# Kernel optimization log

Measured on AMD Instinct MI355X. Metric: run time of the kernel, lower is better.

## Reference

```python
import jax, jax.numpy as jnp
import numpy as np
from functools import partial

IM_H, IM_W = 1024, 1024
PRE_NMS = 1000
POST_NMS = 1000
FPN_POST_NMS = 1000
NMS_THRESH = 0.7
MIN_SIZE = 0.0
XFORM_CLIP = float(np.log(1000.0 / 16.0))  # BoxCoder bbox_xform_clip
K_MIN, K_MAX, K0, S0 = 2, 5, 4, 224.0      # ROI->FPN level mapper
NEG_INF = -1.0e30
N_IMG = 8


def _make_anchors(H, W, stride, n_img):
    """Grid anchors in H,W,A order (matches permute(0,2,3,1) flattening)."""
    ratios = np.array([0.5, 1.0, 2.0])
    size = stride * 8.0
    ws = size * np.sqrt(1.0 / ratios)
    hs = size * np.sqrt(ratios)
    sx = (np.arange(W) + 0.5) * stride
    sy = (np.arange(H) + 0.5) * stride
    cx, cy = np.meshgrid(sx, sy)  # [H,W]
    x1 = cx[..., None] - ws / 2.0
    y1 = cy[..., None] - hs / 2.0
    x2 = cx[..., None] + ws / 2.0
    y2 = cy[..., None] + hs / 2.0
    anc = np.stack([x1, y1, x2, y2], -1).reshape(-1, 4).astype(np.float32)
    return jnp.asarray(np.broadcast_to(anc, (n_img,) + anc.shape).copy())


def setup_inputs() -> dict:
    key = jax.random.key(0)
    ks = jax.random.split(key, 6)
    inp = {
        "obj_p2": jax.random.normal(ks[0], (N_IMG, 3, 256, 256), jnp.float32),
        "obj_p3": jax.random.normal(ks[1], (N_IMG, 3, 128, 128), jnp.float32),
        "obj_p4": jax.random.normal(ks[2], (N_IMG, 3, 64, 64), jnp.float32),
        "breg_p2": jax.random.normal(ks[3], (N_IMG, 12, 256, 256), jnp.float32) * 0.25,
        "breg_p3": jax.random.normal(ks[4], (N_IMG, 12, 128, 128), jnp.float32) * 0.25,
        "breg_p4": jax.random.normal(ks[5], (N_IMG, 12, 64, 64), jnp.float32) * 0.25,
        "anchors_p2": _make_anchors(256, 256, 4, N_IMG),
        "anchors_p3": _make_anchors(128, 128, 8, N_IMG),
        "anchors_p4": _make_anchors(64, 64, 16, N_IMG),
    }
    return inp


def _decode(deltas, anchors):
    # BoxCoder(weights=(1,1,1,1)) decode with the detectron +1 convention
    w = anchors[..., 2] - anchors[..., 0] + 1.0
    h = anchors[..., 3] - anchors[..., 1] + 1.0
    cx = anchors[..., 0] + 0.5 * w
    cy = anchors[..., 1] + 0.5 * h
    dx, dy = deltas[..., 0], deltas[..., 1]
    dw = jnp.minimum(deltas[..., 2], XFORM_CLIP)
    dh = jnp.minimum(deltas[..., 3], XFORM_CLIP)
    pcx = dx * w + cx
    pcy = dy * h + cy
    pw = jnp.exp(dw) * w
    ph = jnp.exp(dh) * h
    return jnp.stack(
        [pcx - 0.5 * pw, pcy - 0.5 * ph, pcx + 0.5 * pw - 1.0, pcy + 0.5 * ph - 1.0], -1
    )


def _nms_keep(boxes, valid, thresh):
    # boxes [K,4] already sorted by score desc; greedy hard NMS -> keep mask
    x1, y1, x2, y2 = boxes[:, 0], boxes[:, 1], boxes[:, 2], boxes[:, 3]
    areas = (x2 - x1 + 1.0) * (y2 - y1 + 1.0)
    xx1 = jnp.maximum(x1[:, None], x1[None, :])
    yy1 = jnp.maximum(y1[:, None], y1[None, :])
    xx2 = jnp.minimum(x2[:, None], x2[None, :])
    yy2 = jnp.minimum(y2[:, None], y2[None, :])
    inter = jnp.clip(xx2 - xx1 + 1.0, 0.0) * jnp.clip(yy2 - yy1 + 1.0, 0.0)
    iou = inter / (areas[:, None] + areas[None, :] - inter)
    K = boxes.shape[0]
    js = jnp.arange(K)

    def body(i, keep):
        sup = keep[i] & (iou[i] > thresh) & (js > i)
        return keep & ~sup

    return jax.lax.fori_loop(0, K, body, valid)


def _per_level(obj, breg, anchors):
    N, A, H, W = obj.shape
    scores = jax.nn.sigmoid(obj.transpose(0, 2, 3, 1).reshape(N, -1))  # [N, HWA]
    deltas = breg.reshape(N, A, 4, H, W).transpose(0, 3, 4, 1, 2).reshape(N, -1, 4)
    k = min(PRE_NMS, scores.shape[1])
    s, idx = jax.lax.top_k(scores, k)  # sorted desc
    d = jnp.take_along_axis(deltas, idx[..., None], axis=1)
    a = jnp.take_along_axis(anchors, idx[..., None], axis=1)
    p = _decode(d, a)
    # clip to image (width-1 / height-1)
    p = jnp.stack(
        [
            jnp.clip(p[..., 0], 0.0, IM_W - 1.0),
            jnp.clip(p[..., 1], 0.0, IM_H - 1.0),
            jnp.clip(p[..., 2], 0.0, IM_W - 1.0),
            jnp.clip(p[..., 3], 0.0, IM_H - 1.0),
        ],
        -1,
    )
    ws = p[..., 2] - p[..., 0] + 1.0
    hs = p[..., 3] - p[..., 1] + 1.0
    xc = p[..., 0] + ws / 2.0
    yc = p[..., 1] + hs / 2.0
    valid = (ws >= MIN_SIZE) & (hs >= MIN_SIZE) & (xc < IM_W) & (yc < IM_H)
    keep = jax.vmap(partial(_nms_keep, thresh=NMS_THRESH))(p, valid)
    ms = jnp.where(keep, s, NEG_INF)
    s2, i2 = jax.lax.top_k(ms, min(POST_NMS, k))
    b2 = jnp.take_along_axis(p, i2[..., None], axis=1)
    return b2, s2


def reference(obj_p2, obj_p3, obj_p4, breg_p2, breg_p3, breg_p4,
              anchors_p2, anchors_p3, anchors_p4):
    levels_in = [
        (obj_p2, breg_p2, anchors_p2),
        (obj_p3, breg_p3, anchors_p3),
        (obj_p4, breg_p4, anchors_p4),
    ]
    bs, ss = zip(*[_per_level(o, b, a) for o, b, a in levels_in])
    boxes = jnp.concatenate(bs, axis=1)   # [N, L*POST_NMS, 4]
    scores = jnp.concatenate(ss, axis=1)  # [N, L*POST_NMS]
    pk = min(FPN_POST_NMS, scores.shape[1])
    fs, fi = jax.lax.top_k(scores, pk)    # per-image inference-mode topk
    fb = jnp.take_along_axis(boxes, fi[..., None], axis=1)
    # ROI -> FPN level mapping
    area = (fb[..., 2] - fb[..., 0] + 1.0) * (fb[..., 3] - fb[..., 1] + 1.0)
    lvl = jnp.floor(K0 + jnp.log2(jnp.sqrt(area) / S0 + 1e-6))
    lvl = jnp.clip(lvl, K_MIN, K_MAX).astype(jnp.int32)
    return fb, fs, lvl
```

## Files before the change

### kernel.cpp

```cpp
#include <hip/hip_runtime.h>

#define NTASK 24
#define KSEL 1000
#define NIMG 8
#define NEG_INF_D (-1e30)
#define SEG 192
#define SORTN 2048


static __device__ __forceinline__ unsigned fkey(float x) {
    unsigned u = __float_as_uint(x);
    return u ^ ((u >> 31) ? 0xFFFFFFFFu : 0x80000000u);
}

static __device__ __forceinline__ float fkey_inv(unsigned key) {
    unsigned u = (key >> 31) ? (key ^ 0x80000000u) : ~key;
    return __uint_as_float(u);
}

static __device__ __forceinline__ unsigned long long dkey(double d) {
    unsigned long long u = (unsigned long long)__double_as_longlong(d);
    if (u >> 63) u = ~u; else u |= 0x8000000000000000ull;
    return u;
}

static __device__ __forceinline__ int level_hw(int lvl) {
    return lvl == 0 ? 65536 : (lvl == 1 ? 16384 : 4096);
}


__global__ __launch_bounds__(256) void k_zero(uint4* __restrict__ p, int n16) {
    const int t = blockIdx.x * 256 + threadIdx.x;
    if (t < n16) p[t] = make_uint4(0u, 0u, 0u, 0u);
}


__global__ __launch_bounds__(256) void k_hist(const float* __restrict__ o2,
                                              const float* __restrict__ o3,
                                              const float* __restrict__ o4,
                                              unsigned* __restrict__ hist) {
    const int task = blockIdx.x, img = task / 3, lvl = task % 3;
    const float* obj = lvl == 0 ? o2 : (lvl == 1 ? o3 : o4);
    const int HW = level_hw(lvl);
    const int total = 3 * HW;
    const float* base = obj + (size_t)img * total;
    const int tid = threadIdx.x;

    __shared__ unsigned h[4096];
    for (int t = tid; t < 4096; t += 256) h[t] = 0u;
    __syncthreads();

    const int per4 = (total / 32) >> 2;
    const int beg4 = blockIdx.y * per4;
    const float4* base4 = (const float4*)base;
    for (int t = beg4 + tid; t < beg4 + per4; t += 256) {
        float4 v = base4[t];
        atomicAdd(&h[fkey(v.x) >> 20], 1u);
        atomicAdd(&h[fkey(v.y) >> 20], 1u);
        atomicAdd(&h[fkey(v.z) >> 20], 1u);
        atomicAdd(&h[fkey(v.w) >> 20], 1u);
    }
    __syncthreads();

    unsigned* H = hist + task * 4096;
    for (int t = tid; t < 4096; t += 256)
        if (h[t]) atomicAdd(&H[t], h[t]);
}


__global__ __launch_bounds__(256) void k_compact(const float* __restrict__ o2,
                                                 const float* __restrict__ o3,
                                                 const float* __restrict__ o4,
                                                 const unsigned* __restrict__ hist,
                                                 int* __restrict__ cntB,
                                                 unsigned long long* __restrict__ cand) {
    const int task = blockIdx.x, img = task / 3, lvl = task % 3;
    const float* obj = lvl == 0 ? o2 : (lvl == 1 ? o3 : o4);
    const int HW = level_hw(lvl);
    const int total = 3 * HW;
    const float* base = obj + (size_t)img * total;
    const int tid = threadIdx.x;

    __shared__ unsigned h[4096];
    __shared__ unsigned part[256];
    __shared__ int sBin;
    __shared__ unsigned long long buf[256];
    __shared__ unsigned scnt;

    const unsigned* H = hist + task * 4096;
    for (int t = tid; t < 4096; t += 256) h[t] = H[t];
    if (tid == 0) scnt = 0u;
    __syncthreads();
    unsigned sacc = 0;
    for (int q = 0; q < 16; ++q) sacc += h[tid * 16 + q];
    part[tid] = sacc;
    __syncthreads();
    if (tid == 0) {
        unsigned cum = 0;
        int c = 255;
        for (; c >= 0; --c) {
            if (cum + part[c] >= (unsigned)KSEL) break;
            cum += part[c];
        }
        if (c < 0) c = 0;
        int bin = 0;
        for (int b = c * 16 + 15; b >= c * 16; --b) {
            if (cum + h[b] >= (unsigned)KSEL) { bin = b; break; }
            cum += h[b];
        }
        sBin = bin;
    }
    __syncthreads();
    const unsigned B = (unsigned)sBin;

    const int per4 = (total / 32) >> 2;
    const int beg4 = blockIdx.y * per4;
    const float4* base4 = (const float4*)base;
    for (int t = beg4 + tid; t < beg4 + per4; t += 256) {
        float4 v = base4[t];
        const int e0 = t * 4;
#pragma unroll
        for (int q = 0; q < 4; ++q) {
            float x = q == 0 ? v.x : (q == 1 ? v.y : (q == 2 ? v.z : v.w));
            unsigned key = fkey(x);
            if ((key >> 20) >= B) {
                unsigned s = atomicAdd(&scnt, 1u);
                if (s < 256u) {
                    int el = e0 + q;
                    int a = el / HW, pos = el - a * HW;
                    int i = pos * 3 + a;
                    buf[s] = ((unsigned long long)key << 32) | (unsigned)(~(unsigned)i);
                }
            }
        }
    }
    __syncthreads();
    int n = (int)scnt; if (n > SEG) n = SEG;
    const int seg = task * 32 + blockIdx.y;
    if (tid == 0) cntB[seg] = n;
    unsigned long long* C = cand + (size_t)seg * SEG;
    for (int t = tid; t < n; t += 256) C[t] = buf[t];
}


__global__ __launch_bounds__(1024) void k_sel(const int* __restrict__ cntB,
                                              const unsigned long long* __restrict__ cand,
                                              unsigned long long* __restrict__ sorted64) {
    const int task = blockIdx.x, tid = threadIdx.x;
    const int wid = tid >> 6, lane = tid & 63;
    __shared__ unsigned long long comp[SORTN];
    __shared__ int pref[33];

    if (tid == 0) {
        int p = 0;
        for (int s = 0; s < 32; ++s) { pref[s] = p; p += cntB[task * 32 + s]; }
        pref[32] = p;
    }
    for (int t = tid; t < SORTN; t += 1024) comp[t] = 0ull;
    __syncthreads();

    for (int s = wid; s < 32; s += 16) {
        const int b = pref[s], n = pref[s + 1] - b;
        const unsigned long long* C = cand + (size_t)(task * 32 + s) * SEG;
        for (int k = lane; k < n; k += 64)
            if (b + k < SORTN) comp[b + k] = C[k];
    }
    __syncthreads();

    for (unsigned k = 2; k <= SORTN; k <<= 1) {
        for (unsigned j = k >> 1; j > 0; j >>= 1) {
            for (unsigned i = tid; i < SORTN; i += 1024) {
                unsigned ixj = i ^ j;
                if (ixj > i) {
                    unsigned long long A = comp[i], Bv = comp[ixj];
                    bool desc = ((i & k) == 0);
                    if ((A < Bv) == desc) { comp[i] = Bv; comp[ixj] = A; }
                }
            }
            __syncthreads();
        }
    }

    for (int t = tid; t < KSEL; t += 1024) sorted64[task * KSEL + t] = comp[t];
}


__global__ __launch_bounds__(128) void k_decode(
    const unsigned long long* __restrict__ sorted64,
    const float* __restrict__ g2, const float* __restrict__ g3, const float* __restrict__ g4,
    const float* __restrict__ a2, const float* __restrict__ a3, const float* __restrict__ a4,
    double* __restrict__ boxes, double* __restrict__ score, int* __restrict__ valid) {

    const int task = blockIdx.x, img = task / 3, lvl = task % 3;
    const int r = blockIdx.y * 125 + threadIdx.x;
    if (threadIdx.x >= 125) return;

    const float* brg = lvl == 0 ? g2 : (lvl == 1 ? g3 : g4);
    const float* anc = lvl == 0 ? a2 : (lvl == 1 ? a3 : a4);
    const int HW = level_hw(lvl);
    const int N = HW * 3;
    const double XC = 4.135166556742356;

    unsigned long long e = sorted64[task * KSEL + r];
    unsigned key = (unsigned)(e >> 32);
    int i = (int)(~(unsigned)(e & 0xFFFFFFFFull));
    int a = i % 3, pos = i / 3;

    double x = (double)fkey_inv(key);
    double s = 1.0 / (1.0 + exp(-x));

    const float* bb = brg + (size_t)img * 12 * HW + (size_t)(a * 4) * HW + pos;
    double dx = (double)bb[0];
    double dy = (double)bb[(size_t)HW];
    double dw = (double)bb[(size_t)2 * HW];
    double dh = (double)bb[(size_t)3 * HW];

    const float* an = anc + ((size_t)img * N + (size_t)i) * 4;
    double ax1 = an[0], ay1 = an[1], ax2 = an[2], ay2 = an[3];

    double w = ax2 - ax1 + 1.0, h = ay2 - ay1 + 1.0;
    double cx = ax1 + 0.5 * w, cy = ay1 + 0.5 * h;
    if (dw > XC) dw = XC;
    if (dh > XC) dh = XC;
    double pcx = dx * w + cx, pcy = dy * h + cy;
    double pw = exp(dw) * w, ph = exp(dh) * h;
    double x1 = pcx - 0.5 * pw, y1 = pcy - 0.5 * ph;
    double x2 = pcx + 0.5 * pw - 1.0, y2 = pcy + 0.5 * ph - 1.0;
    x1 = fmin(fmax(x1, 0.0), 1023.0);
    y1 = fmin(fmax(y1, 0.0), 1023.0);
    x2 = fmin(fmax(x2, 0.0), 1023.0);
    y2 = fmin(fmax(y2, 0.0), 1023.0);
    double ws_ = x2 - x1 + 1.0, hs_ = y2 - y1 + 1.0;
    double xc = x1 + ws_ / 2.0, yc = y1 + hs_ / 2.0;
    int v = (ws_ >= 0.0) && (hs_ >= 0.0) && (xc < 1024.0) && (yc < 1024.0);

    double* bo = boxes + (size_t)(task * KSEL + r) * 4;
    bo[0] = x1; bo[1] = y1; bo[2] = x2; bo[3] = y2;
    score[task * KSEL + r] = s;
    valid[task * KSEL + r] = v;
}


__global__ __launch_bounds__(512) void k_mask(const double* __restrict__ boxes,
                                              unsigned long long* __restrict__ maskT) {
    const int task = blockIdx.x;
    const int wid = threadIdx.x >> 6, lane = threadIdx.x & 63;
    const int t = blockIdx.y * 8 + wid;
    if (t >= 136) return;
    int I = 0, rem = t;
    while (rem >= 16 - I) { rem -= 16 - I; ++I; }
    const int J = I + rem;

    const double* B = boxes + (size_t)task * KSEL * 4;
    const int j = J * 64 + lane;
    const int jc = j < KSEL ? j : KSEL - 1;
    double jx1 = B[jc * 4 + 0], jy1 = B[jc * 4 + 1];
    double jx2 = B[jc * 4 + 2], jy2 = B[jc * 4 + 3];
    double aj = (jx2 - jx1 + 1.0) * (jy2 - jy1 + 1.0);

    unsigned long long* MT = maskT + (size_t)task * 16000 + (size_t)J * KSEL;
    int iend = I * 64 + 64; if (iend > KSEL) iend = KSEL;
    for (int i = I * 64; i < iend; ++i) {
        double ix1 = B[i * 4 + 0], iy1 = B[i * 4 + 1];
        double ix2 = B[i * 4 + 2], iy2 = B[i * 4 + 3];
        double ai = (ix2 - ix1 + 1.0) * (iy2 - iy1 + 1.0);
        double xx1 = fmax(ix1, jx1), yy1 = fmax(iy1, jy1);
        double xx2 = fmin(ix2, jx2), yy2 = fmin(iy2, jy2);
        double iw = xx2 - xx1 + 1.0; iw = iw > 0.0 ? iw : 0.0;
        double ih = yy2 - yy1 + 1.0; ih = ih > 0.0 ? ih : 0.0;
        double inter = iw * ih;
        double iou = inter / (ai + aj - inter);
        bool sup = (j > i) && (j < KSEL) && (iou > 0.7);
        unsigned long long m = __ballot(sup);
        if (lane == 0) MT[i] = m;
    }
}


__global__ __launch_bounds__(1024) void k_nms(const unsigned long long* __restrict__ maskT,
                                              const int* __restrict__ valid,
                                              const double* __restrict__ score,
                                              int* __restrict__ order, double* __restrict__ s2) {
    const int task = blockIdx.x;
    const int tid = threadIdx.x;
    const int wid = tid >> 6, lane = tid & 63;

    __shared__ unsigned long long Msh[16000];
    __shared__ unsigned long long kws[16];
    __shared__ int prefK[16], prefN[16], totKsh;

    {
        const ulonglong2* MG = (const ulonglong2*)(maskT + (size_t)task * 16000);
        ulonglong2* ML = (ulonglong2*)Msh;
        for (int t = tid; t < 8000; t += 1024) ML[t] = MG[t];
    }
    if (tid < 16) kws[tid] = 0ull;
    __syncthreads();
    if (tid < KSEL && valid[task * KSEL + tid])
        atomicOr(&kws[tid >> 6], 1ull << (tid & 63));
    __syncthreads();

    for (int p = 0; p < 16; ++p) {
        if (p > 0 && wid >= p) {
            unsigned long long kp = kws[p - 1];
            unsigned long long m = ((kp >> lane) & 1ull) ? Msh[wid * KSEL + (p - 1) * 64 + lane] : 0ull;
            if (m) atomicAnd(&kws[wid], ~m);
        }
        if (wid == p) {
            __threadfence_block();
            const int row = p * 64 + lane;
            unsigned long long m = (row < KSEL) ? Msh[p * KSEL + row] : 0ull;
            unsigned long long k = kws[p];
            unsigned long long processed = 0ull;
            while (true) {
                unsigned long long sup = __ballot((m & k) != 0ull);
                unsigned long long rem = k & sup & ~processed;
                if (!rem) break;
                int b = __ffsll((long long)rem) - 1;
                unsigned lo = (unsigned)__builtin_amdgcn_readlane((int)(unsigned)(m & 0xFFFFFFFFull), b);
                unsigned hi = (unsigned)__builtin_amdgcn_readlane((int)(unsigned)(m >> 32), b);
                unsigned long long vict = ((unsigned long long)hi << 32) | lo;
                k &= ~vict;
                processed = (1ull << b) | ((1ull << b) - 1ull);
            }
            if (lane == 0) kws[p] = k;
        }
        __syncthreads();
    }

    if (tid == 0) {
        int pk = 0, pn = 0;
        for (int l = 0; l < 16; ++l) {
            prefK[l] = pk; prefN[l] = pn;
            int limit = KSEL - 64 * l; if (limit > 64) limit = 64;
            int kb = (int)__popcll(kws[l]);
            pk += kb; pn += limit - kb;
        }
        totKsh = pk;
    }
    __syncthreads();

    if (tid < 16) {
        unsigned long long kw = kws[tid];
        int limit = KSEL - 64 * tid; if (limit > 64) limit = 64;
        int ck = prefK[tid], cn = totKsh + prefN[tid];
        for (int b = 0; b < limit; ++b) {
            int jj = tid * 64 + b;
            if ((kw >> b) & 1ull) {
                order[task * KSEL + ck] = jj;
                s2[task * KSEL + ck] = score[task * KSEL + jj];
                ++ck;
            } else {
                order[task * KSEL + cn] = jj;
                s2[task * KSEL + cn] = NEG_INF_D;
                ++cn;
            }
        }
    }
}


__global__ __launch_bounds__(1024) void k_final(const double* __restrict__ boxes,
                                                const double* __restrict__ s2,
                                                const int* __restrict__ order,
                                                float* __restrict__ out) {
    const int img = blockIdx.x;
    const int tid = threadIdx.x;
    __shared__ unsigned long long Mkey[KSEL];
    __shared__ int Mid[KSEL];

    const double* L0 = s2 + (size_t)(img * 3 + 0) * KSEL;
    const double* L1 = s2 + (size_t)(img * 3 + 1) * KSEL;
    const double* L2 = s2 + (size_t)(img * 3 + 2) * KSEL;

    if (tid < KSEL) {
        const int r = tid;
        int lo = 0, hi = r;
        while (lo < hi) {
            int a = (lo + hi) >> 1;
            if (dkey(L0[a]) >= dkey(L1[r - 1 - a])) lo = a + 1; else hi = a;
        }
        int a = lo, b = r - a;
        unsigned long long ka = dkey(L0[a]), kb = dkey(L1[b]);
        if (ka >= kb) { Mkey[r] = ka; Mid[r] = a; }
        else          { Mkey[r] = kb; Mid[r] = 1000 + b; }
    }
    __syncthreads();

    if (tid < KSEL) {
        const int r = tid;
        int lo = 0, hi = r;
        while (lo < hi) {
            int a = (lo + hi) >> 1;
            if (Mkey[a] >= dkey(L2[r - 1 - a])) lo = a + 1; else hi = a;
        }
        int a = lo, b = r - a;
        int e;
        if (a < KSEL && Mkey[a] >= dkey(L2[b])) e = Mid[a];
        else e = 2000 + b;

        int l = e / 1000, rr = e - l * 1000;
        int task = img * 3 + l;
        int pos = order[task * KSEL + rr];
        const double* bo = boxes + (size_t)(task * KSEL + pos) * 4;
        double b0 = bo[0], b1 = bo[1], b2 = bo[2], b3 = bo[3];
        double s = s2[task * KSEL + rr];

        float* fb = out + ((size_t)img * KSEL + r) * 4;
        fb[0] = (float)b0; fb[1] = (float)b1; fb[2] = (float)b2; fb[3] = (float)b3;
        out[8 * KSEL * 4 + img * KSEL + r] = (float)s;

        double area = (b2 - b0 + 1.0) * (b3 - b1 + 1.0);
        double lv = floor(4.0 + log2(sqrt(area) / 224.0 + 1e-6));
        if (!(lv >= 2.0)) lv = 2.0;
        if (lv > 5.0) lv = 5.0;
        out[8 * KSEL * 5 + img * KSEL + r] = (float)lv;
    }
}


extern "C" void kernel_launch(void* const* d_in, const int* in_sizes, int n_in,
                              void* d_out, int out_size, void* d_ws, size_t ws_size,
                              hipStream_t stream) {
    const float* o2 = (const float*)d_in[0];
    const float* o3 = (const float*)d_in[1];
    const float* o4 = (const float*)d_in[2];
    const float* g2 = (const float*)d_in[3];
    const float* g3 = (const float*)d_in[4];
    const float* g4 = (const float*)d_in[5];
    const float* a2 = (const float*)d_in[6];
    const float* a3 = (const float*)d_in[7];
    const float* a4 = (const float*)d_in[8];

    char* ws = (char*)d_ws;
    int*                valid = (int*)(ws + 96000);
    double*             score = (double*)(ws + 192000);
    double*             boxes = (double*)(ws + 384000);
    int*                order = (int*)(ws + 1152000);
    double*             s2    = (double*)(ws + 1248000);
    char*               scr   = ws + 1440000;

    unsigned long long* sorted64 = (unsigned long long*)(ws + 1152000);

    unsigned*           hist  = (unsigned*)(scr + 0);
    int*                cntB  = (int*)(scr + 393216);
    unsigned long long* cand  = (unsigned long long*)(scr + 396288);
    unsigned long long* maskT = (unsigned long long*)scr;

    k_zero<<<96, 256, 0, stream>>>((uint4*)scr, 24576);

    k_hist<<<dim3(NTASK, 32), 256, 0, stream>>>(o2, o3, o4, hist);
    k_compact<<<dim3(NTASK, 32), 256, 0, stream>>>(o2, o3, o4, hist, cntB, cand);
    k_sel<<<NTASK, 1024, 0, stream>>>(cntB, cand, sorted64);
    k_decode<<<dim3(NTASK, 8), 128, 0, stream>>>(sorted64, g2, g3, g4, a2, a3, a4,
                                                 boxes, score, valid);
    k_mask<<<dim3(NTASK, 17), 512, 0, stream>>>(boxes, maskT);
    k_nms<<<NTASK, 1024, 0, stream>>>(maskT, valid, score, order, s2);
    k_final<<<NIMG, 1024, 0, stream>>>(boxes, s2, order, (float*)d_out);
}
```

Baseline: 115.3 us.

## Fuse all pipeline stages into one cooperative persistent kernel with grid syncs

Replaces eight separate kernel launches (zero, histogram, compact, select/sort, decode, IoU mask, NMS, final merge) with a single cooperative kernel of 240 blocks of 1024 threads, separated by grid-wide syncs. The goal is to remove per-launch overhead and inter-kernel gaps, which are a large share of this latency-bound pipeline. The cost is that stages with little parallelism (NMS, final merge) use only a few blocks while the rest sit idle. Grid syncs also carry their own cost, and the large 1024-thread blocks with about 128KB of shared memory limit occupancy in the streaming stages.

```diff
diff --git a/kernel.cpp b/kernel.cpp
--- a/kernel.cpp
+++ b/kernel.cpp
@@ -1,4 +1,7 @@
 #include <hip/hip_runtime.h>
+#include <hip/hip_cooperative_groups.h>
+
+namespace cg = cooperative_groups;
 
 #define NTASK 24
 #define KSEL 1000
@@ -6,6 +9,7 @@
 #define NEG_INF_D (-1e30)
 #define SEG 192
 #define SORTN 2048
+#define NBLK 240
 
 
 static __device__ __forceinline__ unsigned fkey(float x) {
@@ -29,392 +33,393 @@
 }
 
 
-__global__ __launch_bounds__(256) void k_zero(uint4* __restrict__ p, int n16) {
-    const int t = blockIdx.x * 256 + threadIdx.x;
-    if (t < n16) p[t] = make_uint4(0u, 0u, 0u, 0u);
-}
-
-
-__global__ __launch_bounds__(256) void k_hist(const float* __restrict__ o2,
-                                              const float* __restrict__ o3,
-                                              const float* __restrict__ o4,
-                                              unsigned* __restrict__ hist) {
-    const int task = blockIdx.x, img = task / 3, lvl = task % 3;
-    const float* obj = lvl == 0 ? o2 : (lvl == 1 ? o3 : o4);
-    const int HW = level_hw(lvl);
-    const int total = 3 * HW;
-    const float* base = obj + (size_t)img * total;
-    const int tid = threadIdx.x;
-
-    __shared__ unsigned h[4096];
-    for (int t = tid; t < 4096; t += 256) h[t] = 0u;
-    __syncthreads();
-
-    const int per4 = (total / 32) >> 2;
-    const int beg4 = blockIdx.y * per4;
-    const float4* base4 = (const float4*)base;
-    for (int t = beg4 + tid; t < beg4 + per4; t += 256) {
-        float4 v = base4[t];
-        atomicAdd(&h[fkey(v.x) >> 20], 1u);
-        atomicAdd(&h[fkey(v.y) >> 20], 1u);
-        atomicAdd(&h[fkey(v.z) >> 20], 1u);
-        atomicAdd(&h[fkey(v.w) >> 20], 1u);
-    }
-    __syncthreads();
-
-    unsigned* H = hist + task * 4096;
-    for (int t = tid; t < 4096; t += 256)
-        if (h[t]) atomicAdd(&H[t], h[t]);
-}
-
-
-__global__ __launch_bounds__(256) void k_compact(const float* __restrict__ o2,
-                                                 const float* __restrict__ o3,
-                                                 const float* __restrict__ o4,
-                                                 const unsigned* __restrict__ hist,
-                                                 int* __restrict__ cntB,
-                                                 unsigned long long* __restrict__ cand) {
-    const int task = blockIdx.x, img = task / 3, lvl = task % 3;
-    const float* obj = lvl == 0 ? o2 : (lvl == 1 ? o3 : o4);
-    const int HW = level_hw(lvl);
-    const int total = 3 * HW;
-    const float* base = obj + (size_t)img * total;
-    const int tid = threadIdx.x;
-
-    __shared__ unsigned h[4096];
-    __shared__ unsigned part[256];
-    __shared__ int sBin;
-    __shared__ unsigned long long buf[256];
-    __shared__ unsigned scnt;
-
-    const unsigned* H = hist + task * 4096;
-    for (int t = tid; t < 4096; t += 256) h[t] = H[t];
-    if (tid == 0) scnt = 0u;
-    __syncthreads();
-    unsigned sacc = 0;
-    for (int q = 0; q < 16; ++q) sacc += h[tid * 16 + q];
-    part[tid] = sacc;
-    __syncthreads();
-    if (tid == 0) {
-        unsigned cum = 0;
-        int c = 255;
-        for (; c >= 0; --c) {
-            if (cum + part[c] >= (unsigned)KSEL) break;
-            cum += part[c];
-        }
-        if (c < 0) c = 0;
-        int bin = 0;
-        for (int b = c * 16 + 15; b >= c * 16; --b) {
-            if (cum + h[b] >= (unsigned)KSEL) { bin = b; break; }
-            cum += h[b];
-        }
-        sBin = bin;
-    }
-    __syncthreads();
-    const unsigned B = (unsigned)sBin;
-
-    const int per4 = (total / 32) >> 2;
-    const int beg4 = blockIdx.y * per4;
-    const float4* base4 = (const float4*)base;
-    for (int t = beg4 + tid; t < beg4 + per4; t += 256) {
-        float4 v = base4[t];
-        const int e0 = t * 4;
-#pragma unroll
-        for (int q = 0; q < 4; ++q) {
-            float x = q == 0 ? v.x : (q == 1 ? v.y : (q == 2 ? v.z : v.w));
-            unsigned key = fkey(x);
-            if ((key >> 20) >= B) {
-                unsigned s = atomicAdd(&scnt, 1u);
-                if (s < 256u) {
-                    int el = e0 + q;
-                    int a = el / HW, pos = el - a * HW;
-                    int i = pos * 3 + a;
-                    buf[s] = ((unsigned long long)key << 32) | (unsigned)(~(unsigned)i);
-                }
-            }
-        }
-    }
-    __syncthreads();
-    int n = (int)scnt; if (n > SEG) n = SEG;
-    const int seg = task * 32 + blockIdx.y;
-    if (tid == 0) cntB[seg] = n;
-    unsigned long long* C = cand + (size_t)seg * SEG;
-    for (int t = tid; t < n; t += 256) C[t] = buf[t];
-}
-
-
-__global__ __launch_bounds__(1024) void k_sel(const int* __restrict__ cntB,
-                                              const unsigned long long* __restrict__ cand,
-                                              unsigned long long* __restrict__ sorted64) {
-    const int task = blockIdx.x, tid = threadIdx.x;
-    const int wid = tid >> 6, lane = tid & 63;
-    __shared__ unsigned long long comp[SORTN];
-    __shared__ int pref[33];
-
-    if (tid == 0) {
-        int p = 0;
-        for (int s = 0; s < 32; ++s) { pref[s] = p; p += cntB[task * 32 + s]; }
-        pref[32] = p;
-    }
-    for (int t = tid; t < SORTN; t += 1024) comp[t] = 0ull;
-    __syncthreads();
-
-    for (int s = wid; s < 32; s += 16) {
-        const int b = pref[s], n = pref[s + 1] - b;
-        const unsigned long long* C = cand + (size_t)(task * 32 + s) * SEG;
-        for (int k = lane; k < n; k += 64)
-            if (b + k < SORTN) comp[b + k] = C[k];
-    }
-    __syncthreads();
-
-    for (unsigned k = 2; k <= SORTN; k <<= 1) {
-        for (unsigned j = k >> 1; j > 0; j >>= 1) {
-            for (unsigned i = tid; i < SORTN; i += 1024) {
-                unsigned ixj = i ^ j;
-                if (ixj > i) {
-                    unsigned long long A = comp[i], Bv = comp[ixj];
-                    bool desc = ((i & k) == 0);
-                    if ((A < Bv) == desc) { comp[i] = Bv; comp[ixj] = A; }
-                }
-            }
-            __syncthreads();
-        }
-    }
-
-    for (int t = tid; t < KSEL; t += 1024) sorted64[task * KSEL + t] = comp[t];
-}
-
-
-__global__ __launch_bounds__(128) void k_decode(
-    const unsigned long long* __restrict__ sorted64,
+__global__ __launch_bounds__(1024) void k_mega(
+    const float* __restrict__ o2, const float* __restrict__ o3, const float* __restrict__ o4,
     const float* __restrict__ g2, const float* __restrict__ g3, const float* __restrict__ g4,
     const float* __restrict__ a2, const float* __restrict__ a3, const float* __restrict__ a4,
-    double* __restrict__ boxes, double* __restrict__ score, int* __restrict__ valid) {
-
-    const int task = blockIdx.x, img = task / 3, lvl = task % 3;
-    const int r = blockIdx.y * 125 + threadIdx.x;
-    if (threadIdx.x >= 125) return;
-
-    const float* brg = lvl == 0 ? g2 : (lvl == 1 ? g3 : g4);
-    const float* anc = lvl == 0 ? a2 : (lvl == 1 ? a3 : a4);
-    const int HW = level_hw(lvl);
-    const int N = HW * 3;
-    const double XC = 4.135166556742356;
-
-    unsigned long long e = sorted64[task * KSEL + r];
-    unsigned key = (unsigned)(e >> 32);
-    int i = (int)(~(unsigned)(e & 0xFFFFFFFFull));
-    int a = i % 3, pos = i / 3;
-
-    double x = (double)fkey_inv(key);
-    double s = 1.0 / (1.0 + exp(-x));
-
-    const float* bb = brg + (size_t)img * 12 * HW + (size_t)(a * 4) * HW + pos;
-    double dx = (double)bb[0];
-    double dy = (double)bb[(size_t)HW];
-    double dw = (double)bb[(size_t)2 * HW];
-    double dh = (double)bb[(size_t)3 * HW];
-
-    const float* an = anc + ((size_t)img * N + (size_t)i) * 4;
-    double ax1 = an[0], ay1 = an[1], ax2 = an[2], ay2 = an[3];
-
-    double w = ax2 - ax1 + 1.0, h = ay2 - ay1 + 1.0;
-    double cx = ax1 + 0.5 * w, cy = ay1 + 0.5 * h;
-    if (dw > XC) dw = XC;
-    if (dh > XC) dh = XC;
-    double pcx = dx * w + cx, pcy = dy * h + cy;
-    double pw = exp(dw) * w, ph = exp(dh) * h;
-    double x1 = pcx - 0.5 * pw, y1 = pcy - 0.5 * ph;
-    double x2 = pcx + 0.5 * pw - 1.0, y2 = pcy + 0.5 * ph - 1.0;
-    x1 = fmin(fmax(x1, 0.0), 1023.0);
-    y1 = fmin(fmax(y1, 0.0), 1023.0);
-    x2 = fmin(fmax(x2, 0.0), 1023.0);
-    y2 = fmin(fmax(y2, 0.0), 1023.0);
-    double ws_ = x2 - x1 + 1.0, hs_ = y2 - y1 + 1.0;
-    double xc = x1 + ws_ / 2.0, yc = y1 + hs_ / 2.0;
-    int v = (ws_ >= 0.0) && (hs_ >= 0.0) && (xc < 1024.0) && (yc < 1024.0);
-
-    double* bo = boxes + (size_t)(task * KSEL + r) * 4;
-    bo[0] = x1; bo[1] = y1; bo[2] = x2; bo[3] = y2;
-    score[task * KSEL + r] = s;
-    valid[task * KSEL + r] = v;
-}
-
-
-__global__ __launch_bounds__(512) void k_mask(const double* __restrict__ boxes,
-                                              unsigned long long* __restrict__ maskT) {
-    const int task = blockIdx.x;
-    const int wid = threadIdx.x >> 6, lane = threadIdx.x & 63;
-    const int t = blockIdx.y * 8 + wid;
-    if (t >= 136) return;
-    int I = 0, rem = t;
-    while (rem >= 16 - I) { rem -= 16 - I; ++I; }
-    const int J = I + rem;
-
-    const double* B = boxes + (size_t)task * KSEL * 4;
-    const int j = J * 64 + lane;
-    const int jc = j < KSEL ? j : KSEL - 1;
-    double jx1 = B[jc * 4 + 0], jy1 = B[jc * 4 + 1];
-    double jx2 = B[jc * 4 + 2], jy2 = B[jc * 4 + 3];
-    double aj = (jx2 - jx1 + 1.0) * (jy2 - jy1 + 1.0);
-
-    unsigned long long* MT = maskT + (size_t)task * 16000 + (size_t)J * KSEL;
-    int iend = I * 64 + 64; if (iend > KSEL) iend = KSEL;
-    for (int i = I * 64; i < iend; ++i) {
-        double ix1 = B[i * 4 + 0], iy1 = B[i * 4 + 1];
-        double ix2 = B[i * 4 + 2], iy2 = B[i * 4 + 3];
-        double ai = (ix2 - ix1 + 1.0) * (iy2 - iy1 + 1.0);
-        double xx1 = fmax(ix1, jx1), yy1 = fmax(iy1, jy1);
-        double xx2 = fmin(ix2, jx2), yy2 = fmin(iy2, jy2);
-        double iw = xx2 - xx1 + 1.0; iw = iw > 0.0 ? iw : 0.0;
-        double ih = yy2 - yy1 + 1.0; ih = ih > 0.0 ? ih : 0.0;
-        double inter = iw * ih;
-        double iou = inter / (ai + aj - inter);
-        bool sup = (j > i) && (j < KSEL) && (iou > 0.7);
-        unsigned long long m = __ballot(sup);
-        if (lane == 0) MT[i] = m;
-    }
-}
-
-
-__global__ __launch_bounds__(1024) void k_nms(const unsigned long long* __restrict__ maskT,
-                                              const int* __restrict__ valid,
-                                              const double* __restrict__ score,
-                                              int* __restrict__ order, double* __restrict__ s2) {
-    const int task = blockIdx.x;
+    unsigned* __restrict__ hist, int* __restrict__ cntB, unsigned long long* __restrict__ cand,
+    unsigned long long* __restrict__ sorted64,
+    double* __restrict__ boxes, double* __restrict__ score, int* __restrict__ valid,
+    unsigned long long* __restrict__ maskT,
+    int* __restrict__ order, double* __restrict__ s2v,
+    float* __restrict__ out) {
+
+    cg::grid_group grid = cg::this_grid();
     const int tid = threadIdx.x;
-    const int wid = tid >> 6, lane = tid & 63;
-
-    __shared__ unsigned long long Msh[16000];
-    __shared__ unsigned long long kws[16];
-    __shared__ int prefK[16], prefN[16], totKsh;
+    const int bid = blockIdx.x;
+
+    __shared__ unsigned long long U64[16000];
+    __shared__ unsigned long long kwsS[16];
+    __shared__ int prefK[16], prefN[16];
+    __shared__ int prefS[33];
+    __shared__ unsigned scntS;
+    __shared__ int sBin, totK;
 
     {
-        const ulonglong2* MG = (const ulonglong2*)(maskT + (size_t)task * 16000);
-        ulonglong2* ML = (ulonglong2*)Msh;
-        for (int t = tid; t < 8000; t += 1024) ML[t] = MG[t];
-    }
-    if (tid < 16) kws[tid] = 0ull;
-    __syncthreads();
-    if (tid < KSEL && valid[task * KSEL + tid])
-        atomicOr(&kws[tid >> 6], 1ull << (tid & 63));
-    __syncthreads();
-
-    for (int p = 0; p < 16; ++p) {
-        if (p > 0 && wid >= p) {
-            unsigned long long kp = kws[p - 1];
-            unsigned long long m = ((kp >> lane) & 1ull) ? Msh[wid * KSEL + (p - 1) * 64 + lane] : 0ull;
-            if (m) atomicAnd(&kws[wid], ~m);
-        }
-        if (wid == p) {
-            __threadfence_block();
-            const int row = p * 64 + lane;
-            unsigned long long m = (row < KSEL) ? Msh[p * KSEL + row] : 0ull;
-            unsigned long long k = kws[p];
-            unsigned long long processed = 0ull;
-            while (true) {
-                unsigned long long sup = __ballot((m & k) != 0ull);
-                unsigned long long rem = k & sup & ~processed;
-                if (!rem) break;
-                int b = __ffsll((long long)rem) - 1;
-                unsigned lo = (unsigned)__builtin_amdgcn_readlane((int)(unsigned)(m & 0xFFFFFFFFull), b);
-                unsigned hi = (unsigned)__builtin_amdgcn_readlane((int)(unsigned)(m >> 32), b);
-                unsigned long long vict = ((unsigned long long)hi << 32) | lo;
-                k &= ~vict;
-                processed = (1ull << b) | ((1ull << b) - 1ull);
-            }
-            if (lane == 0) kws[p] = k;
-        }
-        __syncthreads();
-    }
-
-    if (tid == 0) {
-        int pk = 0, pn = 0;
-        for (int l = 0; l < 16; ++l) {
-            prefK[l] = pk; prefN[l] = pn;
-            int limit = KSEL - 64 * l; if (limit > 64) limit = 64;
-            int kb = (int)__popcll(kws[l]);
-            pk += kb; pn += limit - kb;
-        }
-        totKsh = pk;
-    }
-    __syncthreads();
-
-    if (tid < 16) {
-        unsigned long long kw = kws[tid];
-        int limit = KSEL - 64 * tid; if (limit > 64) limit = 64;
-        int ck = prefK[tid], cn = totKsh + prefN[tid];
-        for (int b = 0; b < limit; ++b) {
-            int jj = tid * 64 + b;
-            if ((kw >> b) & 1ull) {
-                order[task * KSEL + ck] = jj;
-                s2[task * KSEL + ck] = score[task * KSEL + jj];
-                ++ck;
-            } else {
-                order[task * KSEL + cn] = jj;
-                s2[task * KSEL + cn] = NEG_INF_D;
-                ++cn;
-            }
-        }
-    }
-}
-
-
-__global__ __launch_bounds__(1024) void k_final(const double* __restrict__ boxes,
-                                                const double* __restrict__ s2,
-                                                const int* __restrict__ order,
-                                                float* __restrict__ out) {
-    const int img = blockIdx.x;
-    const int tid = threadIdx.x;
-    __shared__ unsigned long long Mkey[KSEL];
-    __shared__ int Mid[KSEL];
-
-    const double* L0 = s2 + (size_t)(img * 3 + 0) * KSEL;
-    const double* L1 = s2 + (size_t)(img * 3 + 1) * KSEL;
-    const double* L2 = s2 + (size_t)(img * 3 + 2) * KSEL;
-
-    if (tid < KSEL) {
-        const int r = tid;
-        int lo = 0, hi = r;
-        while (lo < hi) {
-            int a = (lo + hi) >> 1;
-            if (dkey(L0[a]) >= dkey(L1[r - 1 - a])) lo = a + 1; else hi = a;
-        }
-        int a = lo, b = r - a;
-        unsigned long long ka = dkey(L0[a]), kb = dkey(L1[b]);
-        if (ka >= kb) { Mkey[r] = ka; Mid[r] = a; }
-        else          { Mkey[r] = kb; Mid[r] = 1000 + b; }
-    }
-    __syncthreads();
-
-    if (tid < KSEL) {
-        const int r = tid;
-        int lo = 0, hi = r;
-        while (lo < hi) {
-            int a = (lo + hi) >> 1;
-            if (Mkey[a] >= dkey(L2[r - 1 - a])) lo = a + 1; else hi = a;
-        }
-        int a = lo, b = r - a;
-        int e;
-        if (a < KSEL && Mkey[a] >= dkey(L2[b])) e = Mid[a];
-        else e = 2000 + b;
-
-        int l = e / 1000, rr = e - l * 1000;
-        int task = img * 3 + l;
-        int pos = order[task * KSEL + rr];
-        const double* bo = boxes + (size_t)(task * KSEL + pos) * 4;
-        double b0 = bo[0], b1 = bo[1], b2 = bo[2], b3 = bo[3];
-        double s = s2[task * KSEL + rr];
-
-        float* fb = out + ((size_t)img * KSEL + r) * 4;
-        fb[0] = (float)b0; fb[1] = (float)b1; fb[2] = (float)b2; fb[3] = (float)b3;
-        out[8 * KSEL * 4 + img * KSEL + r] = (float)s;
-
-        double area = (b2 - b0 + 1.0) * (b3 - b1 + 1.0);
-        double lv = floor(4.0 + log2(sqrt(area) / 224.0 + 1e-6));
-        if (!(lv >= 2.0)) lv = 2.0;
-        if (lv > 5.0) lv = 5.0;
-        out[8 * KSEL * 5 + img * KSEL + r] = (float)lv;
+        int g = bid * 1024 + tid;
+        if (g < NTASK * 4096) hist[g] = 0u;
+    }
+    grid.sync();
+
+    {
+        unsigned* h = (unsigned*)U64;
+        for (int vs = bid; vs < 768; vs += NBLK) {
+            const int task = vs >> 5, sl = vs & 31;
+            const int img = task / 3, lvl = task % 3;
+            const float* obj = lvl == 0 ? o2 : (lvl == 1 ? o3 : o4);
+            const int HW = level_hw(lvl);
+            const int total = 3 * HW;
+            const float* base = obj + (size_t)img * total;
+
+            for (int t = tid; t < 4096; t += 1024) h[t] = 0u;
+            __syncthreads();
+
+            const int per4 = (total / 32) >> 2;
+            const int beg4 = sl * per4;
+            const float4* b4 = (const float4*)base;
+            for (int t = beg4 + tid; t < beg4 + per4; t += 1024) {
+                float4 v = b4[t];
+                atomicAdd(&h[fkey(v.x) >> 20], 1u);
+                atomicAdd(&h[fkey(v.y) >> 20], 1u);
+                atomicAdd(&h[fkey(v.z) >> 20], 1u);
+                atomicAdd(&h[fkey(v.w) >> 20], 1u);
+            }
+            __syncthreads();
+            unsigned* H = hist + task * 4096;
+            for (int t = tid; t < 4096; t += 1024)
+                if (h[t]) atomicAdd(&H[t], h[t]);
+            __syncthreads();
+        }
+    }
+    grid.sync();
+
+    {
+        unsigned* h = (unsigned*)U64;
+        unsigned* part = (unsigned*)(U64 + 2048);
+        unsigned long long* buf = U64 + 2304;
+        for (int vs = bid; vs < 768; vs += NBLK) {
+            const int task = vs >> 5, sl = vs & 31;
+            const int img = task / 3, lvl = task % 3;
+            const float* obj = lvl == 0 ? o2 : (lvl == 1 ? o3 : o4);
+            const int HW = level_hw(lvl);
+            const int total = 3 * HW;
+            const float* base = obj + (size_t)img * total;
+
+            const unsigned* H = hist + task * 4096;
+            for (int t = tid; t < 4096; t += 1024) h[t] = H[t];
+            if (tid == 0) scntS = 0u;
+            __syncthreads();
+            if (tid < 256) {
+                unsigned sacc = 0;
+                for (int q = 0; q < 16; ++q) sacc += h[tid * 16 + q];
+                part[tid] = sacc;
+            }
+            __syncthreads();
+            if (tid == 0) {
+                unsigned cum = 0;
+                int c = 255;
+                for (; c >= 0; --c) {
+                    if (cum + part[c] >= (unsigned)KSEL) break;
+                    cum += part[c];
+                }
+                if (c < 0) c = 0;
+                int bin = 0;
+                for (int b = c * 16 + 15; b >= c * 16; --b) {
+                    if (cum + h[b] >= (unsigned)KSEL) { bin = b; break; }
+                    cum += h[b];
+                }
+                sBin = bin;
+            }
+            __syncthreads();
+            const unsigned B = (unsigned)sBin;
+
+            const int per4 = (total / 32) >> 2;
+            const int beg4 = sl * per4;
+            const float4* b4 = (const float4*)base;
+            for (int t = beg4 + tid; t < beg4 + per4; t += 1024) {
+                float4 v = b4[t];
+                const int e0 = t * 4;
+#pragma unroll
+                for (int q = 0; q < 4; ++q) {
+                    float x = q == 0 ? v.x : (q == 1 ? v.y : (q == 2 ? v.z : v.w));
+                    unsigned key = fkey(x);
+                    if ((key >> 20) >= B) {
+                        unsigned s = atomicAdd(&scntS, 1u);
+                        if (s < 256u) {
+                            int el = e0 + q;
+                            int a = el / HW, pos = el - a * HW;
+                            int i = pos * 3 + a;
+                            buf[s] = ((unsigned long long)key << 32) | (unsigned)(~(unsigned)i);
+                        }
+                    }
+                }
+            }
+            __syncthreads();
+            int n = (int)scntS; if (n > SEG) n = SEG;
+            const int seg = task * 32 + sl;
+            if (tid == 0) cntB[seg] = n;
+            unsigned long long* C = cand + (size_t)seg * SEG;
+            for (int t = tid; t < n; t += 1024) C[t] = buf[t];
+            __syncthreads();
+        }
+    }
+    grid.sync();
+
+    if (bid < NTASK) {
+        const int task = bid;
+        const int wid = tid >> 6, lane = tid & 63;
+        unsigned long long* comp = U64;
+
+        if (tid == 0) {
+            int p = 0;
+            for (int s = 0; s < 32; ++s) { prefS[s] = p; p += cntB[task * 32 + s]; }
+            prefS[32] = p;
+        }
+        for (int t = tid; t < SORTN; t += 1024) comp[t] = 0ull;
+        __syncthreads();
+
+        for (int s = wid; s < 32; s += 16) {
+            const int b = prefS[s], n = prefS[s + 1] - b;
+            const unsigned long long* C = cand + (size_t)(task * 32 + s) * SEG;
+            for (int k = lane; k < n; k += 64)
+                if (b + k < SORTN) comp[b + k] = C[k];
+        }
+        __syncthreads();
+
+        for (unsigned k = 2; k <= SORTN; k <<= 1) {
+            for (unsigned j = k >> 1; j > 0; j >>= 1) {
+                for (unsigned i = tid; i < SORTN; i += 1024) {
+                    unsigned ixj = i ^ j;
+                    if (ixj > i) {
+                        unsigned long long A = comp[i], Bv = comp[ixj];
+                        bool desc = ((i & k) == 0);
+                        if ((A < Bv) == desc) { comp[i] = Bv; comp[ixj] = A; }
+                    }
+                }
+                __syncthreads();
+            }
+        }
+
+        for (int t = tid; t < KSEL; t += 1024) sorted64[task * KSEL + t] = comp[t];
+    }
+    grid.sync();
+
+    if (tid < 100) {
+        const int g = bid * 100 + tid;
+        if (g < NTASK * KSEL) {
+            const int task = g / KSEL, r = g - task * KSEL;
+            const int img = task / 3, lvl = task % 3;
+            const float* brg = lvl == 0 ? g2 : (lvl == 1 ? g3 : g4);
+            const float* anc = lvl == 0 ? a2 : (lvl == 1 ? a3 : a4);
+            const int HW = level_hw(lvl);
+            const int N = HW * 3;
+            const double XC = 4.135166556742356;
+
+            unsigned long long e = sorted64[task * KSEL + r];
+            unsigned key = (unsigned)(e >> 32);
+            int i = (int)(~(unsigned)(e & 0xFFFFFFFFull));
+            int a = i % 3, pos = i / 3;
+
+            double x = (double)fkey_inv(key);
+            double s = 1.0 / (1.0 + exp(-x));
+
+            const float* bb = brg + (size_t)img * 12 * HW + (size_t)(a * 4) * HW + pos;
+            double dx = (double)bb[0];
+            double dy = (double)bb[(size_t)HW];
+            double dw = (double)bb[(size_t)2 * HW];
+            double dh = (double)bb[(size_t)3 * HW];
+
+            const float* an = anc + ((size_t)img * N + (size_t)i) * 4;
+            double ax1 = an[0], ay1 = an[1], ax2 = an[2], ay2 = an[3];
+
+            double w = ax2 - ax1 + 1.0, h = ay2 - ay1 + 1.0;
+            double cx = ax1 + 0.5 * w, cy = ay1 + 0.5 * h;
+            if (dw > XC) dw = XC;
+            if (dh > XC) dh = XC;
+            double pcx = dx * w + cx, pcy = dy * h + cy;
+            double pw = exp(dw) * w, ph = exp(dh) * h;
+            double x1 = pcx - 0.5 * pw, y1 = pcy - 0.5 * ph;
+            double x2 = pcx + 0.5 * pw - 1.0, y2 = pcy + 0.5 * ph - 1.0;
+            x1 = fmin(fmax(x1, 0.0), 1023.0);
+            y1 = fmin(fmax(y1, 0.0), 1023.0);
+            x2 = fmin(fmax(x2, 0.0), 1023.0);
+            y2 = fmin(fmax(y2, 0.0), 1023.0);
+            double ws_ = x2 - x1 + 1.0, hs_ = y2 - y1 + 1.0;
+            double xc = x1 + ws_ / 2.0, yc = y1 + hs_ / 2.0;
+            int v = (ws_ >= 0.0) && (hs_ >= 0.0) && (xc < 1024.0) && (yc < 1024.0);
+
+            double* bo = boxes + (size_t)(task * KSEL + r) * 4;
+            bo[0] = x1; bo[1] = y1; bo[2] = x2; bo[3] = y2;
+            score[task * KSEL + r] = s;
+            valid[task * KSEL + r] = v;
+        }
+    }
+    grid.sync();
+
+    {
+        const int wid = tid >> 6, lane = tid & 63;
+        const int tile = bid * 16 + wid;
+        if (tile < NTASK * 136) {
+            const int task = tile / 136;
+            int I = 0, rem = tile - task * 136;
+            while (rem >= 16 - I) { rem -= 16 - I; ++I; }
+            const int J = I + rem;
+
+            const double* B = boxes + (size_t)task * KSEL * 4;
+            const int j = J * 64 + lane;
+            const int jc = j < KSEL ? j : KSEL - 1;
+            double jx1 = B[jc * 4 + 0], jy1 = B[jc * 4 + 1];
+            double jx2 = B[jc * 4 + 2], jy2 = B[jc * 4 + 3];
+            double aj = (jx2 - jx1 + 1.0) * (jy2 - jy1 + 1.0);
+
+            unsigned long long* MT = maskT + (size_t)task * 16000 + (size_t)J * KSEL;
+            int iend = I * 64 + 64; if (iend > KSEL) iend = KSEL;
+            for (int i = I * 64; i < iend; ++i) {
+                double ix1 = B[i * 4 + 0], iy1 = B[i * 4 + 1];
+                double ix2 = B[i * 4 + 2], iy2 = B[i * 4 + 3];
+                double ai = (ix2 - ix1 + 1.0) * (iy2 - iy1 + 1.0);
+                double xx1 = fmax(ix1, jx1), yy1 = fmax(iy1, jy1);
+                double xx2 = fmin(ix2, jx2), yy2 = fmin(iy2, jy2);
+                double iw = xx2 - xx1 + 1.0; iw = iw > 0.0 ? iw : 0.0;
+                double ih = yy2 - yy1 + 1.0; ih = ih > 0.0 ? ih : 0.0;
+                double inter = iw * ih;
+                double iou = inter / (ai + aj - inter);
+                bool sup = (j > i) && (j < KSEL) && (iou > 0.7);
+                unsigned long long m = __ballot(sup);
+                if (lane == 0) MT[i] = m;
+            }
+        }
+    }
+    grid.sync();
+
+    if (bid < NTASK) {
+        const int task = bid;
+        const int wid = tid >> 6, lane = tid & 63;
+        unsigned long long* Msh = U64;
+
+        {
+            const ulonglong2* MG = (const ulonglong2*)(maskT + (size_t)task * 16000);
+            ulonglong2* ML = (ulonglong2*)Msh;
+            for (int t = tid; t < 8000; t += 1024) ML[t] = MG[t];
+        }
+        if (tid < 16) kwsS[tid] = 0ull;
+        __syncthreads();
+        if (tid < KSEL && valid[task * KSEL + tid])
+            atomicOr(&kwsS[tid >> 6], 1ull << (tid & 63));
+        __syncthreads();
+
+        for (int p = 0; p < 16; ++p) {
+            if (p > 0 && wid >= p) {
+                unsigned long long kp = kwsS[p - 1];
+                unsigned long long m = ((kp >> lane) & 1ull) ? Msh[wid * KSEL + (p - 1) * 64 + lane] : 0ull;
+                if (m) atomicAnd(&kwsS[wid], ~m);
+            }
+            if (wid == p) {
+                __threadfence_block();
+                const int row = p * 64 + lane;
+                unsigned long long m = (row < KSEL) ? Msh[p * KSEL + row] : 0ull;
+                unsigned long long k = kwsS[p];
+                unsigned long long processed = 0ull;
+                while (true) {
+                    unsigned long long sup = __ballot((m & k) != 0ull);
+                    unsigned long long rem = k & sup & ~processed;
+                    if (!rem) break;
+                    int b = __ffsll((long long)rem) - 1;
+                    unsigned lo = (unsigned)__builtin_amdgcn_readlane((int)(unsigned)(m & 0xFFFFFFFFull), b);
+                    unsigned hi = (unsigned)__builtin_amdgcn_readlane((int)(unsigned)(m >> 32), b);
+                    unsigned long long vict = ((unsigned long long)hi << 32) | lo;
+                    k &= ~vict;
+                    processed = (1ull << b) | ((1ull << b) - 1ull);
+                }
+                if (lane == 0) kwsS[p] = k;
+            }
+            __syncthreads();
+        }
+
+        if (tid == 0) {
+            int pk = 0, pn = 0;
+            for (int l = 0; l < 16; ++l) {
+                prefK[l] = pk; prefN[l] = pn;
+                int limit = KSEL - 64 * l; if (limit > 64) limit = 64;
+                int kb = (int)__popcll(kwsS[l]);
+                pk += kb; pn += limit - kb;
+            }
+            totK = pk;
+        }
+        __syncthreads();
+
+        if (tid < 16) {
+            unsigned long long kw = kwsS[tid];
+            int limit = KSEL - 64 * tid; if (limit > 64) limit = 64;
+            int ck = prefK[tid], cn = totK + prefN[tid];
+            for (int b = 0; b < limit; ++b) {
+                int jj = tid * 64 + b;
+                if ((kw >> b) & 1ull) {
+                    order[task * KSEL + ck] = jj;
+                    s2v[task * KSEL + ck] = score[task * KSEL + jj];
+                    ++ck;
+                } else {
+                    order[task * KSEL + cn] = jj;
+                    s2v[task * KSEL + cn] = NEG_INF_D;
+                    ++cn;
+                }
+            }
+        }
+    }
+    grid.sync();
+
+    if (bid < NIMG) {
+        const int img = bid;
+        unsigned long long* Mkey = U64;
+        int* Mid = (int*)(U64 + 1000);
+
+        const double* L0 = s2v + (size_t)(img * 3 + 0) * KSEL;
+        const double* L1 = s2v + (size_t)(img * 3 + 1) * KSEL;
+        const double* L2 = s2v + (size_t)(img * 3 + 2) * KSEL;
+
+        if (tid < KSEL) {
+            const int r = tid;
+            int lo = 0, hi = r;
+            while (lo < hi) {
+                int a = (lo + hi) >> 1;
+                if (dkey(L0[a]) >= dkey(L1[r - 1 - a])) lo = a + 1; else hi = a;
+            }
+            int a = lo, b = r - a;
+            unsigned long long ka = dkey(L0[a]), kb = dkey(L1[b]);
+            if (ka >= kb) { Mkey[r] = ka; Mid[r] = a; }
+            else          { Mkey[r] = kb; Mid[r] = 1000 + b; }
+        }
+        __syncthreads();
+
+        if (tid < KSEL) {
+            const int r = tid;
+            int lo = 0, hi = r;
+            while (lo < hi) {
+                int a = (lo + hi) >> 1;
+                if (Mkey[a] >= dkey(L2[r - 1 - a])) lo = a + 1; else hi = a;
+            }
+            int a = lo, b = r - a;
+            int e;
+            if (a < KSEL && Mkey[a] >= dkey(L2[b])) e = Mid[a];
+            else e = 2000 + b;
+
+            int l = e / 1000, rr = e - l * 1000;
+            int task = img * 3 + l;
+            int pos = order[task * KSEL + rr];
+            const double* bo = boxes + (size_t)(task * KSEL + pos) * 4;
+            double b0 = bo[0], b1 = bo[1], b2 = bo[2], b3 = bo[3];
+            double s = s2v[task * KSEL + rr];
+
+            float* fb = out + ((size_t)img * KSEL + r) * 4;
+            fb[0] = (float)b0; fb[1] = (float)b1; fb[2] = (float)b2; fb[3] = (float)b3;
+            out[8 * KSEL * 4 + img * KSEL + r] = (float)s;
+
+            double area = (b2 - b0 + 1.0) * (b3 - b1 + 1.0);
+            double lv = floor(4.0 + log2(sqrt(area) / 224.0 + 1e-6));
+            if (!(lv >= 2.0)) lv = 2.0;
+            if (lv > 5.0) lv = 5.0;
+            out[8 * KSEL * 5 + img * KSEL + r] = (float)lv;
+        }
     }
 }
 
@@ -441,20 +446,23 @@
     char*               scr   = ws + 1440000;
 
     unsigned long long* sorted64 = (unsigned long long*)(ws + 1152000);
-
     unsigned*           hist  = (unsigned*)(scr + 0);
     int*                cntB  = (int*)(scr + 393216);
     unsigned long long* cand  = (unsigned long long*)(scr + 396288);
     unsigned long long* maskT = (unsigned long long*)scr;
 
-    k_zero<<<96, 256, 0, stream>>>((uint4*)scr, 24576);
-
-    k_hist<<<dim3(NTASK, 32), 256, 0, stream>>>(o2, o3, o4, hist);
-    k_compact<<<dim3(NTASK, 32), 256, 0, stream>>>(o2, o3, o4, hist, cntB, cand);
-    k_sel<<<NTASK, 1024, 0, stream>>>(cntB, cand, sorted64);
-    k_decode<<<dim3(NTASK, 8), 128, 0, stream>>>(sorted64, g2, g3, g4, a2, a3, a4,
-                                                 boxes, score, valid);
-    k_mask<<<dim3(NTASK, 17), 512, 0, stream>>>(boxes, maskT);
-    k_nms<<<NTASK, 1024, 0, stream>>>(maskT, valid, score, order, s2);
-    k_final<<<NIMG, 1024, 0, stream>>>(boxes, s2, order, (float*)d_out);
-}
+    float* outp = (float*)d_out;
+
+    void* args[] = {
+        (void*)&o2, (void*)&o3, (void*)&o4,
+        (void*)&g2, (void*)&g3, (void*)&g4,
+        (void*)&a2, (void*)&a3, (void*)&a4,
+        (void*)&hist, (void*)&cntB, (void*)&cand,
+        (void*)&sorted64,
+        (void*)&boxes, (void*)&score, (void*)&valid,
+        (void*)&maskT,
+        (void*)&order, (void*)&s2,
+        (void*)&outp
+    };
+    hipLaunchCooperativeKernel((void*)k_mega, dim3(NBLK), dim3(1024), args, 0, stream);
+}
```

New measurement: 303.8 us. 163% more time.

## Fuse histogram and compaction into one kernel with redundant per-block histograms

Applied to the files above, without the earlier changes.

Merges the zero, histogram and compact kernels into a single kernel. Each of 4 blocks per task builds the full task histogram in shared memory on its own, instead of combining partial histograms through global atomics. This removes two launches, the global histogram round trip and the zeroing pass. In exchange every block reads the whole level again (4x redundant reads of the objectness data), and the largest level's histogram is done by only 24x4 blocks, which may leave much of the GPU idle.

```diff
diff --git a/kernel.cpp b/kernel.cpp
--- a/kernel.cpp
+++ b/kernel.cpp
@@ -4,7 +4,8 @@
 #define KSEL 1000
 #define NIMG 8
 #define NEG_INF_D (-1e30)
-#define SEG 192
+#define NSEG 4
+#define SEGCAP 2048
 #define SORTN 2048
 
 
@@ -29,17 +30,12 @@
 }
 
 
-__global__ __launch_bounds__(256) void k_zero(uint4* __restrict__ p, int n16) {
-    const int t = blockIdx.x * 256 + threadIdx.x;
-    if (t < n16) p[t] = make_uint4(0u, 0u, 0u, 0u);
-}
-
-
-__global__ __launch_bounds__(256) void k_hist(const float* __restrict__ o2,
-                                              const float* __restrict__ o3,
-                                              const float* __restrict__ o4,
-                                              unsigned* __restrict__ hist) {
-    const int task = blockIdx.x, img = task / 3, lvl = task % 3;
+__global__ __launch_bounds__(1024) void k_histcompact(
+    const float* __restrict__ o2, const float* __restrict__ o3, const float* __restrict__ o4,
+    int* __restrict__ cntB, unsigned long long* __restrict__ cand) {
+
+    const int task = blockIdx.x, quarter = blockIdx.y;
+    const int img = task / 3, lvl = task % 3;
     const float* obj = lvl == 0 ? o2 : (lvl == 1 ? o3 : o4);
     const int HW = level_hw(lvl);
     const int total = 3 * HW;
@@ -47,14 +43,19 @@
     const int tid = threadIdx.x;
 
     __shared__ unsigned h[4096];
-    for (int t = tid; t < 4096; t += 256) h[t] = 0u;
-    __syncthreads();
-
-    const int per4 = (total / 32) >> 2;
-    const int beg4 = blockIdx.y * per4;
-    const float4* base4 = (const float4*)base;
-    for (int t = beg4 + tid; t < beg4 + per4; t += 256) {
-        float4 v = base4[t];
+    __shared__ unsigned part[256];
+    __shared__ int sBin;
+    __shared__ unsigned long long buf[SEGCAP];
+    __shared__ unsigned scnt;
+
+    for (int t = tid; t < 4096; t += 1024) h[t] = 0u;
+    if (tid == 0) scnt = 0u;
+    __syncthreads();
+
+    const int total4 = total >> 2;
+    const float4* b4 = (const float4*)base;
+    for (int t = tid; t < total4; t += 1024) {
+        float4 v = b4[t];
         atomicAdd(&h[fkey(v.x) >> 20], 1u);
         atomicAdd(&h[fkey(v.y) >> 20], 1u);
         atomicAdd(&h[fkey(v.z) >> 20], 1u);
@@ -62,38 +63,11 @@
     }
     __syncthreads();
 
-    unsigned* H = hist + task * 4096;
-    for (int t = tid; t < 4096; t += 256)
-        if (h[t]) atomicAdd(&H[t], h[t]);
-}
-
-
-__global__ __launch_bounds__(256) void k_compact(const float* __restrict__ o2,
-                                                 const float* __restrict__ o3,
-                                                 const float* __restrict__ o4,
-                                                 const unsigned* __restrict__ hist,
-                                                 int* __restrict__ cntB,
-                                                 unsigned long long* __restrict__ cand) {
-    const int task = blockIdx.x, img = task / 3, lvl = task % 3;
-    const float* obj = lvl == 0 ? o2 : (lvl == 1 ? o3 : o4);
-    const int HW = level_hw(lvl);
-    const int total = 3 * HW;
-    const float* base = obj + (size_t)img * total;
-    const int tid = threadIdx.x;
-
-    __shared__ unsigned h[4096];
-    __shared__ unsigned part[256];
-    __shared__ int sBin;
-    __shared__ unsigned long long buf[256];
-    __shared__ unsigned scnt;
-
-    const unsigned* H = hist + task * 4096;
-    for (int t = tid; t < 4096; t += 256) h[t] = H[t];
-    if (tid == 0) scnt = 0u;
-    __syncthreads();
-    unsigned sacc = 0;
-    for (int q = 0; q < 16; ++q) sacc += h[tid * 16 + q];
-    part[tid] = sacc;
+    if (tid < 256) {
+        unsigned sacc = 0;
+        for (int q = 0; q < 16; ++q) sacc += h[tid * 16 + q];
+        part[tid] = sacc;
+    }
     __syncthreads();
     if (tid == 0) {
         unsigned cum = 0;
@@ -113,11 +87,10 @@
     __syncthreads();
     const unsigned B = (unsigned)sBin;
 
-    const int per4 = (total / 32) >> 2;
-    const int beg4 = blockIdx.y * per4;
-    const float4* base4 = (const float4*)base;
-    for (int t = beg4 + tid; t < beg4 + per4; t += 256) {
-        float4 v = base4[t];
+    const int qper4 = total4 >> 2;
+    const int beg4 = quarter * qper4;
+    for (int t = beg4 + tid; t < beg4 + qper4; t += 1024) {
+        float4 v = b4[t];
         const int e0 = t * 4;
 #pragma unroll
         for (int q = 0; q < 4; ++q) {
@@ -125,7 +98,7 @@
             unsigned key = fkey(x);
             if ((key >> 20) >= B) {
                 unsigned s = atomicAdd(&scnt, 1u);
-                if (s < 256u) {
+                if (s < (unsigned)SEGCAP) {
                     int el = e0 + q;
                     int a = el / HW, pos = el - a * HW;
                     int i = pos * 3 + a;
@@ -135,11 +108,11 @@
         }
     }
     __syncthreads();
-    int n = (int)scnt; if (n > SEG) n = SEG;
-    const int seg = task * 32 + blockIdx.y;
+    int n = (int)scnt; if (n > SEGCAP) n = SEGCAP;
+    const int seg = task * NSEG + quarter;
     if (tid == 0) cntB[seg] = n;
-    unsigned long long* C = cand + (size_t)seg * SEG;
-    for (int t = tid; t < n; t += 256) C[t] = buf[t];
+    unsigned long long* C = cand + (size_t)seg * SEGCAP;
+    for (int t = tid; t < n; t += 1024) C[t] = buf[t];
 }
 
 
@@ -149,19 +122,19 @@
     const int task = blockIdx.x, tid = threadIdx.x;
     const int wid = tid >> 6, lane = tid & 63;
     __shared__ unsigned long long comp[SORTN];
-    __shared__ int pref[33];
+    __shared__ int pref[NSEG + 1];
 
     if (tid == 0) {
         int p = 0;
-        for (int s = 0; s < 32; ++s) { pref[s] = p; p += cntB[task * 32 + s]; }
-        pref[32] = p;
+        for (int s = 0; s < NSEG; ++s) { pref[s] = p; p += cntB[task * NSEG + s]; }
+        pref[NSEG] = p;
     }
     for (int t = tid; t < SORTN; t += 1024) comp[t] = 0ull;
     __syncthreads();
 
-    for (int s = wid; s < 32; s += 16) {
+    for (int s = wid; s < NSEG; s += 16) {
         const int b = pref[s], n = pref[s + 1] - b;
-        const unsigned long long* C = cand + (size_t)(task * 32 + s) * SEG;
+        const unsigned long long* C = cand + (size_t)(task * NSEG + s) * SEGCAP;
         for (int k = lane; k < n; k += 64)
             if (b + k < SORTN) comp[b + k] = C[k];
     }
@@ -442,15 +415,11 @@
 
     unsigned long long* sorted64 = (unsigned long long*)(ws + 1152000);
 
-    unsigned*           hist  = (unsigned*)(scr + 0);
-    int*                cntB  = (int*)(scr + 393216);
-    unsigned long long* cand  = (unsigned long long*)(scr + 396288);
+    int*                cntB  = (int*)(scr + 0);
+    unsigned long long* cand  = (unsigned long long*)(scr + 1024);
     unsigned long long* maskT = (unsigned long long*)scr;
 
-    k_zero<<<96, 256, 0, stream>>>((uint4*)scr, 24576);
-
-    k_hist<<<dim3(NTASK, 32), 256, 0, stream>>>(o2, o3, o4, hist);
-    k_compact<<<dim3(NTASK, 32), 256, 0, stream>>>(o2, o3, o4, hist, cntB, cand);
+    k_histcompact<<<dim3(NTASK, NSEG), 1024, 0, stream>>>(o2, o3, o4, cntB, cand);
     k_sel<<<NTASK, 1024, 0, stream>>>(cntB, cand, sorted64);
     k_decode<<<dim3(NTASK, 8), 128, 0, stream>>>(sorted64, g2, g3, g4, a2, a3, a4,
                                                  boxes, score, valid);
```

New measurement: 126.6 us. 1.1x slower.
